# Kernel optimization log

Measured on AMD Instinct MI355X. Metric: run time of the kernel, lower is better.

## Reference

```python
import jax, jax.numpy as jnp
import numpy as np

B, P, TL = 2, 256, 1280          # batch, prefix len, text len
H, HEADS, HD = 1024, 16, 64      # hidden, heads, head_dim
NL, V = 2, 32000                 # layers, vocab


def layernorm(x, g, b, eps=1e-5):
    mu = jnp.mean(x, axis=-1, keepdims=True)
    var = jnp.mean((x - mu) ** 2, axis=-1, keepdims=True)
    return (x - mu) / jnp.sqrt(var + eps) * g + b


def setup_inputs() -> dict:
    key = jax.random.key(0)
    ks = jax.random.split(key, 12)
    s = 0.02
    return {
        "prefix_embeds": jax.random.normal(ks[0], (B, P, H), jnp.float32),
        "text_ids": jax.random.randint(ks[1], (B, TL), 0, V),
        "embed": jax.random.normal(ks[2], (V, H), jnp.float32) * s,
        "Wq": jax.random.normal(ks[3], (NL, H, H), jnp.float32) * s,
        "Wk": jax.random.normal(ks[4], (NL, H, H), jnp.float32) * s,
        "Wv": jax.random.normal(ks[5], (NL, H, H), jnp.float32) * s,
        "Wo": jax.random.normal(ks[6], (NL, H, H), jnp.float32) * s,
        "g1": jnp.ones((NL, H), jnp.float32),
        "b1": jnp.zeros((NL, H), jnp.float32),
        "g2": jnp.ones((NL, H), jnp.float32),
        "b2": jnp.zeros((NL, H), jnp.float32),
        "W1": jax.random.normal(ks[7], (NL, H, 4 * H), jnp.float32) * s,
        "bm1": jnp.zeros((NL, 4 * H), jnp.float32),
        "W2": jax.random.normal(ks[8], (NL, 4 * H, H), jnp.float32) * s,
        "bm2": jnp.zeros((NL, H), jnp.float32),
        "gf": jnp.ones((H,), jnp.float32),
        "bf": jnp.zeros((H,), jnp.float32),
        "Whead": jax.random.normal(ks[9], (H, V), jnp.float32) * s,
    }


def reference(prefix_embeds, text_ids, embed, Wq, Wk, Wv, Wo,
              g1, b1, g2, b2, W1, bm1, W2, bm2, gf, bf, Whead):
    x = jnp.concatenate([prefix_embeds, embed[text_ids]], axis=1)  # [B,T,H]
    T = x.shape[1]
    causal = jnp.tril(jnp.ones((T, T), dtype=bool))                # True = keep
    scale = 1.0 / jnp.sqrt(jnp.float32(HD))
    for l in range(NL):
        h = layernorm(x, g1[l], b1[l])
        q = (h @ Wq[l]).reshape(B, T, HEADS, HD).transpose(0, 2, 1, 3)
        k = (h @ Wk[l]).reshape(B, T, HEADS, HD).transpose(0, 2, 1, 3)
        v = (h @ Wv[l]).reshape(B, T, HEADS, HD).transpose(0, 2, 1, 3)
        scores = jnp.einsum('bhqd,bhkd->bhqk', q, k) * scale       # [B,h,T,T]
        scores = jnp.where(causal, scores, -jnp.inf)
        attn = jax.nn.softmax(scores, axis=-1)
        out = jnp.einsum('bhqk,bhkd->bhqd', attn, v)
        out = out.transpose(0, 2, 1, 3).reshape(B, T, H) @ Wo[l]
        x = x + out
        h2 = layernorm(x, g2[l], b2[l])
        x = x + jax.nn.silu(h2 @ W1[l] + bm1[l]) @ W2[l] + bm2[l]
    x = layernorm(x, gf, bf)
    return x @ Whead                                               # [B,T,V]
```

## Files before the change

kernel.cpp:

```cpp
#include <hip/hip_runtime.h>
#include <stdint.h>

#define B_ 2
#define P_ 256
#define TL_ 1280
#define T_ 1536
#define H_ 1024
#define HEADS_ 16
#define HD_ 64
#define NL_ 2
#define V_ 32000
#define F_ 4096
#define BT_ (B_ * T_)

typedef __attribute__((ext_vector_type(4))) float f32x4;
typedef __attribute__((ext_vector_type(8))) short short8;
typedef __attribute__((ext_vector_type(4))) short short4v;

typedef __attribute__((address_space(3))) uint32_t lds_u32_t;
typedef const __attribute__((address_space(1))) uint32_t glb_u32_t;

__device__ inline void gload_lds16(const void* g, void* l) {
    __builtin_amdgcn_global_load_lds((glb_u32_t*)g, (lds_u32_t*)l, 16, 0, 0);
}

__device__ inline short f2bf(float f) {
    union { float f; unsigned u; } v; v.f = f;
    unsigned r = v.u + 0x7FFF + ((v.u >> 16) & 1);
    return (short)(r >> 16);
}

#define BAR() asm volatile("s_barrier" ::: "memory")
#define WAIT_VM0() asm volatile("s_waitcnt vmcnt(0)" ::: "memory")
#define WAIT_VM4() asm volatile("s_waitcnt vmcnt(4)" ::: "memory")
#define WAIT_VM8() asm volatile("s_waitcnt vmcnt(8)" ::: "memory")

__global__ __launch_bounds__(256) void k_cvt_all(
    const float* __restrict__ Wq, const float* __restrict__ Wk,
    const float* __restrict__ Wv, const float* __restrict__ Wo,
    const float* __restrict__ W1, const float* __restrict__ W2,
    const float* __restrict__ Wh,
    short* __restrict__ WqkvT, short* __restrict__ WoT,
    short* __restrict__ W1T, short* __restrict__ W2T, short* __restrict__ WhT) {
    int id = blockIdx.x;
    const float* src;
    short* dst;
    int K, N;
    float scale = 1.f;
    if (id < 6144) {
        int mat = id >> 10;
        int tile = id & 1023;
        int l = mat / 3, which = mat - l * 3;
        src = (which == 0 ? Wq : which == 1 ? Wk : Wv) + (size_t)l * H_ * H_;
        dst = WqkvT + (size_t)(l * 3 + which) * H_ * H_;
        K = H_; N = H_;
        if (which == 0) scale = 0.125f;
        id = tile;
    } else if (id < 8192) {
        int rel = id - 6144;
        int l = rel >> 10;
        src = Wo + (size_t)l * H_ * H_;
        dst = WoT + (size_t)l * H_ * H_;
        K = H_; N = H_;
        id = rel & 1023;
    } else if (id < 16384) {
        int rel = id - 8192;
        int l = rel >> 12;
        src = W1 + (size_t)l * H_ * F_;
        dst = W1T + (size_t)l * H_ * F_;
        K = H_; N = F_;
        id = rel & 4095;
    } else if (id < 24576) {
        int rel = id - 16384;
        int l = rel >> 12;
        src = W2 + (size_t)l * F_ * H_;
        dst = W2T + (size_t)l * F_ * H_;
        K = F_; N = H_;
        id = rel & 4095;
    } else {
        id -= 24576;
        src = Wh; dst = WhT;
        K = H_; N = V_;
    }
    int ntn = N >> 5;
    int nb = (id % ntn) * 32, kb = (id / ntn) * 32;

    __shared__ float ts[32][36];
    int tid = threadIdx.x;
    int r = tid >> 3, c4 = (tid & 7) * 4;
    f32x4 v = __builtin_nontemporal_load((const f32x4*)&src[(size_t)(kb + r) * N + nb + c4]);
    *(f32x4*)&ts[r][c4] = v;
    __syncthreads();
    int wn = tid >> 3, wk4 = (tid & 7) * 4;
    short o[4];
#pragma unroll
    for (int j = 0; j < 4; ++j) o[j] = f2bf(ts[wk4 + j][wn] * scale);
    *(short4v*)&dst[(size_t)(nb + wn) * K + kb + wk4] = *(short4v*)o;
}

__global__ __launch_bounds__(256) void k_embed_ln(const float* __restrict__ prefix,
                                                  const int* __restrict__ ids,
                                                  const float* __restrict__ emb,
                                                  const float* __restrict__ g,
                                                  const float* __restrict__ b,
                                                  float* __restrict__ x,
                                                  short* __restrict__ h) {
    int r = blockIdx.x;
    int bb = r / T_, t = r % T_;
    const float* src = (t < P_) ? (prefix + (size_t)(bb * P_ + t) * H_)
                                : (emb + (size_t)ids[bb * TL_ + (t - P_)] * H_);
    int tid = threadIdx.x;
    f32x4 v = *(const f32x4*)&src[tid * 4];
    *(f32x4*)&x[(size_t)r * H_ + tid * 4] = v;
    float s = v[0] + v[1] + v[2] + v[3];
    float sq = v[0] * v[0] + v[1] * v[1] + v[2] * v[2] + v[3] * v[3];
#pragma unroll
    for (int off = 32; off; off >>= 1) {
        s += __shfl_down(s, off, 64);
        sq += __shfl_down(sq, off, 64);
    }
    __shared__ float red[10];
    int wid = tid >> 6;
    if ((tid & 63) == 0) { red[wid] = s; red[4 + wid] = sq; }
    __syncthreads();
    if (tid == 0) {
        float S = red[0] + red[1] + red[2] + red[3];
        float SQ = red[4] + red[5] + red[6] + red[7];
        float mu = S * (1.0f / H_);
        float var = SQ * (1.0f / H_) - mu * mu;
        red[8] = mu;
        red[9] = rsqrtf(var + 1e-5f);
    }
    __syncthreads();
    float mu = red[8], rstd = red[9];
    short o[4];
#pragma unroll
    for (int j = 0; j < 4; ++j)
        o[j] = f2bf((v[j] - mu) * rstd * g[tid * 4 + j] + b[tid * 4 + j]);
    *(short4v*)&h[(size_t)r * H_ + tid * 4] = *(short4v*)o;
}

__global__ __launch_bounds__(256) void k_add_ln(float* __restrict__ x,
                                                const float* __restrict__ p,
                                                const float* __restrict__ g,
                                                const float* __restrict__ b,
                                                short* __restrict__ out) {
    int r = blockIdx.x;
    int tid = threadIdx.x;
    size_t base = (size_t)r * H_ + tid * 4;
    f32x4 v = *(f32x4*)&x[base];
#pragma unroll
    for (int sl = 0; sl < 4; ++sl) {
        f32x4 a = *(const f32x4*)&p[(size_t)sl * BT_ * H_ + base];
#pragma unroll
        for (int j = 0; j < 4; ++j) v[j] += a[j];
    }
    *(f32x4*)&x[base] = v;
    float s = v[0] + v[1] + v[2] + v[3];
    float sq = v[0] * v[0] + v[1] * v[1] + v[2] * v[2] + v[3] * v[3];
#pragma unroll
    for (int off = 32; off; off >>= 1) {
        s += __shfl_down(s, off, 64);
        sq += __shfl_down(sq, off, 64);
    }
    __shared__ float red[10];
    int wid = tid >> 6;
    if ((tid & 63) == 0) { red[wid] = s; red[4 + wid] = sq; }
    __syncthreads();
    if (tid == 0) {
        float S = red[0] + red[1] + red[2] + red[3];
        float SQ = red[4] + red[5] + red[6] + red[7];
        float mu = S * (1.0f / H_);
        float var = SQ * (1.0f / H_) - mu * mu;
        red[8] = mu;
        red[9] = rsqrtf(var + 1e-5f);
    }
    __syncthreads();
    float mu = red[8], rstd = red[9];
    short o[4];
#pragma unroll
    for (int j = 0; j < 4; ++j)
        o[j] = f2bf((v[j] - mu) * rstd * g[tid * 4 + j] + b[tid * 4 + j]);
    *(short4v*)&out[base] = *(short4v*)o;
}

template <int STORE, bool HAS_BIAS, bool SILU, int NSPLIT>
__global__ __launch_bounds__(256) void k_gemm(const short* __restrict__ A,
                                              const short* __restrict__ Bt,
                                              const float* __restrict__ bias,
                                              void* __restrict__ outp,
                                              void* __restrict__ outp2,
                                              void* __restrict__ outp3,
                                              int M, int N, int K, float alpha) {
    __shared__ short As[4][128 * 32];
    __shared__ short Bs[4][128 * 32];
    int tid = threadIdx.x;
    int lane = tid & 63, w = tid >> 6;
    int wr = w >> 1, wc = w & 1;
    int nwg = gridDim.x;
    int mblocks = M >> 7;
    int cpx = nwg >> 3;
    int logical = (blockIdx.x & 7) * cpx + (blockIdx.x >> 3);
    int ks = 0;
    if (NSPLIT > 1) {
        int per = mblocks * (N >> 7);
        ks = logical / per;
        logical -= ks * per;
    }
    int rp = logical % mblocks, cp = logical / mblocks;
    int mbase = rp * 128, nbase = cp * 128;
    int Kh = K / NSPLIT;
    int lr = lane & 15, hi = lane >> 4;
    int lg = hi * 4;

    f32x4 acc[4][4] = {};

    int r0 = tid >> 2;
    int gcol = ((tid & 3) ^ (r0 & 3)) * 8;
    const short* Ab = A + (size_t)mbase * K + (size_t)ks * Kh;
    const short* Bb = Bt + (size_t)nbase * K + (size_t)ks * Kh;

    int koff = ((hi ^ (lr & 3)) << 4);
    int arow[4], brow[4];
#pragma unroll
    for (int m = 0; m < 4; ++m) arow[m] = (wr * 64 + m * 16 + lr) * 64;
#pragma unroll
    for (int n = 0; n < 4; ++n) brow[n] = (wc * 64 + n * 16 + lr) * 64;

    auto stage = [&](int t, int buf) {
        const short* ga = Ab + (size_t)r0 * K + t * 32 + gcol;
        const short* gb = Bb + (size_t)r0 * K + t * 32 + gcol;
        char* la = (char*)&As[buf][0];
        char* lb = (char*)&Bs[buf][0];
        gload_lds16(ga, la + tid * 16);
        gload_lds16(ga + (size_t)64 * K, la + tid * 16 + 4096);
        gload_lds16(gb, lb + tid * 16);
        gload_lds16(gb + (size_t)64 * K, lb + tid * 16 + 4096);
    };

    int NT = Kh >> 5;
    stage(0, 0);
    stage(1, 1);
    stage(2, 2);
    WAIT_VM8();
    BAR();

    for (int t = 0; t < NT; ++t) {
        bool iss = (t + 3 < NT);
        if (iss) stage(t + 3, (t + 3) & 3);
        const char* a = (const char*)&As[t & 3][0];
        const char* b = (const char*)&Bs[t & 3][0];
        short8 af[4], bfr[4];
#pragma unroll
        for (int mi = 0; mi < 4; ++mi) af[mi] = *(const short8*)(a + arow[mi] + koff);
#pragma unroll
        for (int ni = 0; ni < 4; ++ni) bfr[ni] = *(const short8*)(b + brow[ni] + koff);
        __builtin_amdgcn_s_setprio(1);
#pragma unroll
        for (int mi = 0; mi < 4; ++mi)
#pragma unroll
            for (int ni = 0; ni < 4; ++ni)
                acc[mi][ni] = __builtin_amdgcn_mfma_f32_16x16x32_bf16(af[mi], bfr[ni], acc[mi][ni], 0, 0, 0);
        __builtin_amdgcn_s_setprio(0);
        if (t + 1 < NT) {
            if (iss) WAIT_VM8();
            else if (t + 2 < NT) WAIT_VM4();
            else WAIT_VM0();
            BAR();
        }
    }

#pragma unroll
    for (int ni = 0; ni < 4; ++ni) {
        int col = nbase + wc * 64 + ni * 16 + lr;
        float bv = (HAS_BIAS && ks == 0) ? bias[col] : 0.f;
#pragma unroll
        for (int mi = 0; mi < 4; ++mi) {
#pragma unroll
            for (int j = 0; j < 4; ++j) {
                int row = mbase + wr * 64 + mi * 16 + lg + j;
                float vv = acc[mi][ni][j] * alpha + bv;
                if (SILU) vv = vv / (1.f + __expf(-vv));
                if (STORE == 0) {
                    ((float*)outp)[(size_t)ks * M * N + (size_t)row * N + col] = vv;
                } else if (STORE == 1) {
                    ((short*)outp)[(size_t)row * N + col] = f2bf(vv);
                } else {
                    int seg = col >> 10;
                    int c = col & 1023;
                    if (seg == 0) {
                        ((short*)outp)[(size_t)row * H_ + c] = f2bf(vv);
                    } else if (seg == 1) {
                        ((short*)outp2)[(size_t)row * H_ + c] = f2bf(vv);
                    } else {
                        int bb = row / T_, t2 = row % T_;
                        ((short*)outp3)[((size_t)(bb * HEADS_ + (c >> 6)) * HD_ + (c & 63)) * T_ + t2] = f2bf(vv);
                    }
                }
            }
        }
    }
}

__global__ __launch_bounds__(512, 2) void k_gemm8(const short* __restrict__ A,
                                                  const short* __restrict__ Bt,
                                                  float* __restrict__ C,
                                                  int M, int N, int K) {
    __shared__ short As[2 * 256 * 64];
    __shared__ short Bs[2 * 256 * 64];
    int tid = threadIdx.x;
    int lane = tid & 63, w = tid >> 6;
    int wr = w >> 2, wc = w & 3;
    int lr = lane & 15, hi = lane >> 4;

    int mtiles = M >> 8;
    int total = mtiles * (N >> 8);
    int g = ((blockIdx.x & 7) << 5) + (blockIdx.x >> 3);
    int qq = total >> 8, rr = total & 255;
    int start = g * qq + (g < rr ? g : rr);
    int cnt = qq + (g < rr ? 1 : 0);

    int r0 = tid >> 3;
    int gcol = ((tid & 7) ^ (r0 & 7)) * 8;
    int koff0 = (hi * 16) ^ ((lr & 7) << 4);
    int koff1 = (64 + hi * 16) ^ ((lr & 7) << 4);
    int arow[8], brow[4];
#pragma unroll
    for (int m = 0; m < 8; ++m) arow[m] = (wr * 128 + m * 16 + lr) * 128;
#pragma unroll
    for (int n = 0; n < 4; ++n) brow[n] = (wc * 64 + n * 16 + lr) * 128;

    f32x4 acc[8][4];
    short8 aF[4][2], bF[4][2];
    const char* Ac = (const char*)As;
    const char* Bc = (const char*)Bs;

    auto stage = [&](const short* Gb, char* Lb, int tau, int hf) {
        const short* g0 = Gb + (size_t)(hf * 128 + r0) * K + tau * 64 + gcol;
        char* l = Lb + (tau & 1) * 32768 + hf * 16384;
        gload_lds16(g0, l + tid * 16);
        gload_lds16(g0 + (size_t)64 * K, l + (tid + 512) * 16);
    };
    auto prolog = [&](const short* Ab, const short* Bb) {
        stage(Ab, (char*)As, 0, 0); stage(Ab, (char*)As, 0, 1);
        stage(Bb, (char*)Bs, 0, 0); stage(Bb, (char*)Bs, 0, 1);
        stage(Ab, (char*)As, 1, 0); stage(Ab, (char*)As, 1, 1);
        stage(Bb, (char*)Bs, 1, 0); stage(Bb, (char*)Bs, 1, 1);
    };
    auto lda4 = [&](const char* base, int roff) {
#pragma unroll
        for (int m = 0; m < 4; ++m) {
            aF[m][0] = *(const short8*)(base + arow[roff + m] + koff0);
            aF[m][1] = *(const short8*)(base + arow[roff + m] + koff1);
        }
    };
    auto ldb2 = [&](const char* base, int noff) {
#pragma unroll
        for (int n = 0; n < 2; ++n) {
            bF[noff + n][0] = *(const short8*)(base + brow[noff + n] + koff0);
            bF[noff + n][1] = *(const short8*)(base + brow[noff + n] + koff1);
        }
    };

#define MFMA_QUAD(MOFF, NOFF)                                                          \
    __builtin_amdgcn_s_setprio(1);                                                     \
    _Pragma("unroll") for (int m = 0; m < 4; ++m) {                                    \
        _Pragma("unroll") for (int n = 0; n < 2; ++n) {                                \
            acc[MOFF + m][NOFF + n] = __builtin_amdgcn_mfma_f32_16x16x32_bf16(         \
                aF[m][0], bF[NOFF + n][0], acc[MOFF + m][NOFF + n], 0, 0, 0);          \
            acc[MOFF + m][NOFF + n] = __builtin_amdgcn_mfma_f32_16x16x32_bf16(         \
                aF[m][1], bF[NOFF + n][1], acc[MOFF + m][NOFF + n], 0, 0, 0);          \
        }                                                                              \
    }                                                                                  \
    __builtin_amdgcn_s_setprio(0);

    int NK = K >> 6;
    int niters = NK >> 1;

    for (int i = 0; i < cnt; ++i) {
        int t0 = start + i;
        int rp = t0 % mtiles, cp = t0 / mtiles;
        const short* Ab = A + (size_t)rp * 256 * K;
        const short* Bb = Bt + (size_t)cp * 256 * K;
        f32x4 zz = {0.f, 0.f, 0.f, 0.f};
#pragma unroll
        for (int m = 0; m < 8; ++m)
#pragma unroll
            for (int n = 0; n < 4; ++n) acc[m][n] = zz;

        if (i == 0) {
            prolog(Ab, Bb);
            WAIT_VM0();
            BAR();
        }

        for (int it = 0; it < niters; ++it) {
            bool st = it < niters - 1;
            int u2 = 2 * it + 2, v2 = 2 * it + 3;
            const char* a0 = Ac;            const char* b0 = Bc;
            const char* a1 = Ac + 32768;    const char* b1 = Bc + 32768;

            lda4(a0, 0); ldb2(b0, 0);
            BAR();
            MFMA_QUAD(0, 0);
            BAR();
            ldb2(b0, 2);
            BAR();
            MFMA_QUAD(0, 2);
            BAR();
            lda4(a0, 4);
            if (st) stage(Bb, (char*)Bs, u2, 0);
            BAR();
            MFMA_QUAD(4, 0);
            BAR();
            if (st) stage(Bb, (char*)Bs, u2, 1);
            BAR();
            MFMA_QUAD(4, 2);
            if (st) { WAIT_VM4(); } else { WAIT_VM0(); }
            BAR();

            lda4(a1, 0); ldb2(b1, 0);
            if (st) stage(Ab, (char*)As, u2, 0);
            BAR();
            MFMA_QUAD(0, 0);
            BAR();
            ldb2(b1, 2);
            if (st) stage(Ab, (char*)As, u2, 1);
            BAR();
            MFMA_QUAD(0, 2);
            BAR();
            lda4(a1, 4);
            if (st) stage(Bb, (char*)Bs, v2, 0);
            BAR();
            MFMA_QUAD(4, 0);
            BAR();
            if (st) { stage(Bb, (char*)Bs, v2, 1); stage(Ab, (char*)As, v2, 0); stage(Ab, (char*)As, v2, 1); }
            BAR();
            MFMA_QUAD(4, 2);
            if (st) { WAIT_VM8(); } else { WAIT_VM0(); }
            BAR();
        }

        int crow = rp * 256 + wr * 128 + hi * 4;
        int ccol = cp * 256 + wc * 64 + lr;
#pragma unroll
        for (int m = 0; m < 8; ++m)
#pragma unroll
            for (int n = 0; n < 4; ++n) {
#pragma unroll
                for (int j = 0; j < 4; ++j)
                    C[(size_t)(crow + m * 16 + j) * N + ccol + n * 16] = acc[m][n][j];
            }

        if (i + 1 < cnt) {
            int t1 = t0 + 1;
            int rp1 = t1 % mtiles, cp1 = t1 / mtiles;
            prolog(A + (size_t)rp1 * 256 * K, Bt + (size_t)cp1 * 256 * K);
            WAIT_VM0();
            BAR();
        }
    }
#undef MFMA_QUAD
}

__global__ __launch_bounds__(256) void k_attn(const short* __restrict__ q,
                                              const short* __restrict__ k,
                                              const short* __restrict__ vT,
                                              short* __restrict__ out) {
    int qt = (T_ / 64 - 1) - blockIdx.x;
    int head = blockIdx.y, b = blockIdx.z;
    int qbase = qt * 64;
    __shared__ short Qs[64][72];
    __shared__ short Ps[4][16][72];
    int tid = threadIdx.x, lane = tid & 63, w = tid >> 6;
    int lr = lane & 15, lg4 = (lane >> 4) * 4, lk8 = (lane >> 4) * 8;

#pragma unroll
    for (int c = 0; c < 2; ++c) {
        int chunk = tid + 256 * c;
        int row = chunk >> 3, h8 = (chunk & 7) * 8;
        *(short8*)&Qs[row][h8] =
            *(const short8*)&q[(size_t)(b * T_ + qbase + row) * H_ + head * HD_ + h8];
    }
    __syncthreads();

    short8 qf[2];
    qf[0] = *(short8*)&Qs[w * 16 + lr][lk8];
    qf[1] = *(short8*)&Qs[w * 16 + lr][32 + lk8];

    f32x4 o[4] = {};
    float m[4] = {-1e30f, -1e30f, -1e30f, -1e30f};
    float lsum[4] = {0.f, 0.f, 0.f, 0.f};

    for (int kt = 0; kt <= qt; ++kt) {
        int kb = kt * 64;
        f32x4 s[4] = {};
#pragma unroll
        for (int ks = 0; ks < 2; ++ks) {
#pragma unroll
            for (int f = 0; f < 4; ++f) {
                short8 kf = *(const short8*)&k[(size_t)(b * T_ + kb + f * 16 + lr) * H_ +
                                               head * HD_ + ks * 32 + lk8];
                s[f] = __builtin_amdgcn_mfma_f32_16x16x32_bf16(qf[ks], kf, s[f], 0, 0, 0);
            }
        }
        if (kt == qt) {
#pragma unroll
            for (int f = 0; f < 4; ++f) {
                int key = kb + f * 16 + lr;
#pragma unroll
                for (int j = 0; j < 4; ++j) {
                    int qrow = qbase + w * 16 + lg4 + j;
                    if (key > qrow) s[f][j] = -1e30f;
                }
            }
        }
#pragma unroll
        for (int j = 0; j < 4; ++j) {
            float mx = fmaxf(fmaxf(s[0][j], s[1][j]), fmaxf(s[2][j], s[3][j]));
#pragma unroll
            for (int off = 1; off < 16; off <<= 1) mx = fmaxf(mx, __shfl_xor(mx, off, 64));
            float mnew = fmaxf(m[j], mx);
            float sc = __expf(m[j] - mnew);
            m[j] = mnew;
            float rs = 0.f;
#pragma unroll
            for (int f = 0; f < 4; ++f) {
                float p = __expf(s[f][j] - mnew);
                s[f][j] = p;
                rs += p;
            }
#pragma unroll
            for (int off = 1; off < 16; off <<= 1) rs += __shfl_xor(rs, off, 64);
            lsum[j] = lsum[j] * sc + rs;
#pragma unroll
            for (int f = 0; f < 4; ++f) o[f][j] *= sc;
#pragma unroll
            for (int f = 0; f < 4; ++f) Ps[w][lg4 + j][f * 16 + lr] = f2bf(s[f][j]);
        }
#pragma unroll
        for (int ks2 = 0; ks2 < 2; ++ks2) {
            short8 pf = *(short8*)&Ps[w][lr][ks2 * 32 + lk8];
            __builtin_amdgcn_s_setprio(1);
#pragma unroll
            for (int f = 0; f < 4; ++f) {
                short8 vf = *(const short8*)&vT[((size_t)(b * HEADS_ + head) * HD_ + f * 16 + lr) * T_ +
                                                kb + ks2 * 32 + lk8];
                o[f] = __builtin_amdgcn_mfma_f32_16x16x32_bf16(pf, vf, o[f], 0, 0, 0);
            }
            __builtin_amdgcn_s_setprio(0);
        }
    }
#pragma unroll
    for (int f = 0; f < 4; ++f)
#pragma unroll
        for (int j = 0; j < 4; ++j) {
            float val = o[f][j] / lsum[j];
            out[(size_t)(b * T_ + qbase + w * 16 + lg4 + j) * H_ + head * HD_ + f * 16 + lr] =
                f2bf(val);
        }
}

extern "C" void kernel_launch(void* const* d_in, const int* in_sizes, int n_in,
                              void* d_out, int out_size, void* d_ws, size_t ws_size,
                              hipStream_t stream) {
    const float* prefix = (const float*)d_in[0];
    const int* ids = (const int*)d_in[1];
    const float* emb = (const float*)d_in[2];
    const float* Wq = (const float*)d_in[3];
    const float* Wk = (const float*)d_in[4];
    const float* Wv = (const float*)d_in[5];
    const float* Wo = (const float*)d_in[6];
    const float* g1 = (const float*)d_in[7];
    const float* b1 = (const float*)d_in[8];
    const float* g2 = (const float*)d_in[9];
    const float* b2 = (const float*)d_in[10];
    const float* W1 = (const float*)d_in[11];
    const float* bm1 = (const float*)d_in[12];
    const float* W2 = (const float*)d_in[13];
    const float* bm2 = (const float*)d_in[14];
    const float* gf = (const float*)d_in[15];
    const float* bf = (const float*)d_in[16];
    const float* Whead = (const float*)d_in[17];
    float* out = (float*)d_out;

    char* wsp = (char*)d_ws;
    float* x = (float*)wsp;   wsp += (size_t)BT_ * H_ * 4;
    float* p = (float*)wsp;   wsp += (size_t)4 * BT_ * H_ * 4;
    short* h = (short*)wsp;   wsp += (size_t)BT_ * H_ * 2;
    short* qb = (short*)wsp;  wsp += (size_t)BT_ * H_ * 2;
    short* kb = (short*)wsp;  wsp += (size_t)BT_ * H_ * 2;
    short* vT = (short*)wsp;  wsp += (size_t)BT_ * H_ * 2;
    short* ao = (short*)wsp;  wsp += (size_t)BT_ * H_ * 2;
    short* mid = (short*)wsp; wsp += (size_t)BT_ * F_ * 2;
    short* WqkvT = (short*)wsp; wsp += (size_t)NL_ * 3 * H_ * H_ * 2;
    short* WoT = (short*)wsp;   wsp += (size_t)NL_ * H_ * H_ * 2;
    short* W1T = (short*)wsp;   wsp += (size_t)NL_ * H_ * F_ * 2;
    short* W2T = (short*)wsp;   wsp += (size_t)NL_ * F_ * H_ * 2;
    short* WhT = (short*)wsp;   wsp += (size_t)H_ * V_ * 2;

    dim3 blk(256);
    k_cvt_all<<<dim3(56576), blk, 0, stream>>>(Wq, Wk, Wv, Wo, W1, W2, Whead,
                                               WqkvT, WoT, W1T, W2T, WhT);
    k_embed_ln<<<BT_, blk, 0, stream>>>(prefix, ids, emb, g1, b1, x, h);
    for (int l = 0; l < NL_; ++l) {
        size_t o1 = (size_t)l * H_ * H_;
        size_t oq = (size_t)l * 3 * H_ * H_;
        size_t o2 = (size_t)l * H_ * F_;
        k_gemm<3, false, false, 1><<<dim3(576), blk, 0, stream>>>(
            h, WqkvT + oq, nullptr, qb, kb, vT, BT_, 3 * H_, H_, 1.f);
        k_attn<<<dim3(T_ / 64, HEADS_, B_), blk, 0, stream>>>(qb, kb, vT, ao);
        k_gemm<0, false, false, 4><<<dim3(768), blk, 0, stream>>>(
            ao, WoT + o1, nullptr, p, nullptr, nullptr, BT_, H_, H_, 1.f);
        k_add_ln<<<BT_, blk, 0, stream>>>(x, p, g2 + l * H_, b2 + l * H_, h);
        k_gemm<1, true, true, 1><<<dim3(768), blk, 0, stream>>>(
            h, W1T + o2, bm1 + (size_t)l * F_, mid, nullptr, nullptr, BT_, F_, H_, 1.f);
        k_gemm<0, true, false, 4><<<dim3(768), blk, 0, stream>>>(
            mid, W2T + o2, bm2 + (size_t)l * H_, p, nullptr, nullptr, BT_, H_, F_, 1.f);
        const float* gn = (l + 1 < NL_) ? g1 + (l + 1) * H_ : gf;
        const float* bn = (l + 1 < NL_) ? b1 + (l + 1) * H_ : bf;
        k_add_ln<<<BT_, blk, 0, stream>>>(x, p, gn, bn, h);
    }
    k_gemm8<<<dim3(256), dim3(512), 0, stream>>>(h, WhT, out, BT_, V_, H_);
}
```

Before: 974.1 us.

## Deepen GEMM K-tile to 64 with double buffering, LDS-transposed V store, reorder attention tiles

The 128x128 GEMM now stages K=64 per step with an 8-chunk XOR swizzle and two LDS buffers instead of K=32 with four buffers. The V-projection epilogue is staged through LDS so transposed V is written with 16-byte vector stores instead of scattered 2-byte writes. The attention grid no longer processes the longest causal query tiles first. Together these aim to cut barrier count and uncoalesced stores, but the pipeline now waits for all loads each step, which may expose memory latency.

New measurement: 878.7 us. -9.8%, faster.

```diff
diff --git a/kernel.cpp b/kernel.cpp
--- a/kernel.cpp
+++ b/kernel.cpp
@@ -192,8 +192,7 @@
                                               void* __restrict__ outp2,
                                               void* __restrict__ outp3,
                                               int M, int N, int K, float alpha) {
-    __shared__ short As[4][128 * 32];
-    __shared__ short Bs[4][128 * 32];
+    __shared__ short SH[32768];
     int tid = threadIdx.x;
     int lane = tid & 63, w = tid >> 6;
     int wr = w >> 1, wc = w & 1;
@@ -215,59 +214,88 @@
 
     f32x4 acc[4][4] = {};
 
-    int r0 = tid >> 2;
-    int gcol = ((tid & 3) ^ (r0 & 3)) * 8;
     const short* Ab = A + (size_t)mbase * K + (size_t)ks * Kh;
     const short* Bb = Bt + (size_t)nbase * K + (size_t)ks * Kh;
 
-    int koff = ((hi ^ (lr & 3)) << 4);
-    int arow[4], brow[4];
-#pragma unroll
-    for (int m = 0; m < 4; ++m) arow[m] = (wr * 64 + m * 16 + lr) * 64;
-#pragma unroll
-    for (int n = 0; n < 4; ++n) brow[n] = (wc * 64 + n * 16 + lr) * 64;
+    int koffb[2];
+    koffb[0] = ((hi) ^ (lr & 7)) << 4;
+    koffb[1] = ((4 + hi) ^ (lr & 7)) << 4;
+    int arowb[4], browb[4];
+#pragma unroll
+    for (int m = 0; m < 4; ++m) arowb[m] = (wr * 64 + m * 16 + lr) * 128;
+#pragma unroll
+    for (int n = 0; n < 4; ++n) browb[n] = (wc * 64 + n * 16 + lr) * 128;
 
     auto stage = [&](int t, int buf) {
-        const short* ga = Ab + (size_t)r0 * K + t * 32 + gcol;
-        const short* gb = Bb + (size_t)r0 * K + t * 32 + gcol;
-        char* la = (char*)&As[buf][0];
-        char* lb = (char*)&Bs[buf][0];
-        gload_lds16(ga, la + tid * 16);
-        gload_lds16(ga + (size_t)64 * K, la + tid * 16 + 4096);
-        gload_lds16(gb, lb + tid * 16);
-        gload_lds16(gb + (size_t)64 * K, lb + tid * 16 + 4096);
+        short* la = SH + buf * 8192;
+        short* lb = SH + 16384 + buf * 8192;
+#pragma unroll
+        for (int c = 0; c < 4; ++c) {
+            int S = tid + 256 * c;
+            int r = S >> 3, ch = S & 7;
+            int gofs = t * 64 + ((ch ^ (r & 7)) << 3);
+            gload_lds16(Ab + (size_t)r * K + gofs, la + S * 8);
+            gload_lds16(Bb + (size_t)r * K + gofs, lb + S * 8);
+        }
     };
 
-    int NT = Kh >> 5;
+    int NT = Kh >> 6;
     stage(0, 0);
-    stage(1, 1);
-    stage(2, 2);
-    WAIT_VM8();
+    WAIT_VM0();
     BAR();
 
     for (int t = 0; t < NT; ++t) {
-        bool iss = (t + 3 < NT);
-        if (iss) stage(t + 3, (t + 3) & 3);
-        const char* a = (const char*)&As[t & 3][0];
-        const char* b = (const char*)&Bs[t & 3][0];
-        short8 af[4], bfr[4];
-#pragma unroll
-        for (int mi = 0; mi < 4; ++mi) af[mi] = *(const short8*)(a + arow[mi] + koff);
-#pragma unroll
-        for (int ni = 0; ni < 4; ++ni) bfr[ni] = *(const short8*)(b + brow[ni] + koff);
+        if (t + 1 < NT) stage(t + 1, (t + 1) & 1);
+        const char* a = (const char*)(SH + (t & 1) * 8192);
+        const char* b = (const char*)(SH + 16384 + (t & 1) * 8192);
+        short8 af[2][4], bfr[2][4];
+#pragma unroll
+        for (int kk = 0; kk < 2; ++kk) {
+#pragma unroll
+            for (int m = 0; m < 4; ++m) af[kk][m] = *(const short8*)(a + arowb[m] + koffb[kk]);
+#pragma unroll
+            for (int n = 0; n < 4; ++n) bfr[kk][n] = *(const short8*)(b + browb[n] + koffb[kk]);
+        }
         __builtin_amdgcn_s_setprio(1);
 #pragma unroll
-        for (int mi = 0; mi < 4; ++mi)
-#pragma unroll
-            for (int ni = 0; ni < 4; ++ni)
-                acc[mi][ni] = __builtin_amdgcn_mfma_f32_16x16x32_bf16(af[mi], bfr[ni], acc[mi][ni], 0, 0, 0);
+        for (int kk = 0; kk < 2; ++kk)
+#pragma unroll
+            for (int m = 0; m < 4; ++m)
+#pragma unroll
+                for (int n = 0; n < 4; ++n)
+                    acc[m][n] = __builtin_amdgcn_mfma_f32_16x16x32_bf16(af[kk][m], bfr[kk][n], acc[m][n], 0, 0, 0);
         __builtin_amdgcn_s_setprio(0);
         if (t + 1 < NT) {
-            if (iss) WAIT_VM8();
-            else if (t + 2 < NT) WAIT_VM4();
-            else WAIT_VM0();
-            BAR();
-        }
+            WAIT_VM0();
+            BAR();
+        }
+    }
+
+    if (STORE == 3 && nbase >= 2048) {
+        BAR();
+        short* Tt = SH;
+#pragma unroll
+        for (int ni = 0; ni < 4; ++ni) {
+            int c2 = wc * 64 + ni * 16 + lr;
+#pragma unroll
+            for (int mi = 0; mi < 4; ++mi)
+#pragma unroll
+                for (int j = 0; j < 4; ++j)
+                    Tt[c2 * 136 + wr * 64 + mi * 16 + lg + j] = f2bf(acc[mi][ni][j]);
+        }
+        BAR();
+        int c2 = tid >> 1;
+        int half = (tid & 1) * 64;
+        int cc = (nbase + c2) & 1023;
+        int head = cc >> 6, hd = cc & 63;
+        int bb = mbase / T_;
+        int t0 = mbase - bb * T_;
+        short* dst = (short*)outp3 +
+                     ((size_t)(bb * HEADS_ + head) * HD_ + hd) * T_ + t0 + half;
+#pragma unroll
+        for (int r8 = 0; r8 < 8; ++r8)
+            *(short8*)&dst[r8 * 8] = *(short8*)&Tt[c2 * 136 + half + r8 * 8];
+        return;
     }
 
 #pragma unroll
@@ -290,11 +318,8 @@
                     int c = col & 1023;
                     if (seg == 0) {
                         ((short*)outp)[(size_t)row * H_ + c] = f2bf(vv);
-                    } else if (seg == 1) {
+                    } else {
                         ((short*)outp2)[(size_t)row * H_ + c] = f2bf(vv);
-                    } else {
-                        int bb = row / T_, t2 = row % T_;
-                        ((short*)outp3)[((size_t)(bb * HEADS_ + (c >> 6)) * HD_ + (c & 63)) * T_ + t2] = f2bf(vv);
                     }
                 }
             }
@@ -467,8 +492,7 @@
                                               const short* __restrict__ k,
                                               const short* __restrict__ vT,
                                               short* __restrict__ out) {
-    int qt = (T_ / 64 - 1) - blockIdx.x;
-    int head = blockIdx.y, b = blockIdx.z;
+    int qt = blockIdx.x, head = blockIdx.y, b = blockIdx.z;
     int qbase = qt * 64;
     __shared__ short Qs[64][72];
     __shared__ short Ps[4][16][72];
```
